# Performance work log

Hardware: AMD Instinct MI355X
Metric: run time of the kernel (lower is better)

## Reference

```python
import jax, jax.numpy as jnp
import numpy as np

DIM = 128
HEADS = 4
POS_DIM = (DIM // 4) // 4  # DynamicPosBias: pos_dim = (dim//4)//4 = 8


def _layernorm(x, g, b, eps=1e-5):
    m = x.mean(-1, keepdims=True)
    v = x.var(-1, keepdims=True)
    return (x - m) / jnp.sqrt(v + eps) * g + b


def setup_inputs() -> dict:
    key = jax.random.key(0)
    ks = jax.random.split(key, 16)
    B_, N, C = 64, 512, DIM
    s = 0.02
    inp = {
        "x": jax.random.normal(ks[0], (B_, N, C), jnp.float32),
        "y": jax.random.normal(ks[1], (B_, N, C), jnp.float32),
        "H": 8, "W": 8, "D": 8,
        "qkv_w": jax.random.normal(ks[2], (3 * C, C), jnp.float32) * s,
        "qkv_b": jnp.zeros((3 * C,), jnp.float32),
        "proj_w": jax.random.normal(ks[3], (C, C), jnp.float32) * s,
        "proj_b": jnp.zeros((C,), jnp.float32),
        "pos_proj_w": jax.random.normal(ks[4], (POS_DIM, 3), jnp.float32) * s,
        "pos_proj_b": jnp.zeros((POS_DIM,), jnp.float32),
        "ln1_g": jnp.ones((POS_DIM,), jnp.float32),
        "ln1_b": jnp.zeros((POS_DIM,), jnp.float32),
        "p1_w": jax.random.normal(ks[5], (POS_DIM, POS_DIM), jnp.float32) * s,
        "p1_b": jnp.zeros((POS_DIM,), jnp.float32),
        "ln2_g": jnp.ones((POS_DIM,), jnp.float32),
        "ln2_b": jnp.zeros((POS_DIM,), jnp.float32),
        "p2_w": jax.random.normal(ks[6], (POS_DIM, POS_DIM), jnp.float32) * s,
        "p2_b": jnp.zeros((POS_DIM,), jnp.float32),
        "ln3_g": jnp.ones((POS_DIM,), jnp.float32),
        "ln3_b": jnp.zeros((POS_DIM,), jnp.float32),
        "p3_w": jax.random.normal(ks[7], (HEADS, POS_DIM), jnp.float32) * s,
        "p3_b": jnp.zeros((HEADS,), jnp.float32),
    }
    return inp


def _rel_pos_static(H, W, D):
    # biases table: all relative offsets, shape ((2H-1)(2W-1)(2D-1), 3)
    bh = np.arange(1 - H, H)
    bw = np.arange(1 - W, W)
    bd = np.arange(1 - D, D)
    biases = np.stack(np.meshgrid(bh, bw, bd, indexing="ij")).reshape(3, -1).T
    # relative position index, shape (N, N)
    coords = np.stack(np.meshgrid(np.arange(H), np.arange(W), np.arange(D), indexing="ij")).reshape(3, -1)
    rel = coords[:, :, None] - coords[:, None, :]  # (3, N, N)
    rel = rel.transpose(1, 2, 0).astype(np.int64)
    rel[:, :, 0] += H - 1
    rel[:, :, 1] += W - 1
    rel[:, :, 2] += D - 1
    rel[:, :, 0] *= (2 * W - 1) * (2 * D - 1)
    rel[:, :, 1] *= 2 * D - 1
    idx = rel.sum(-1)  # (N, N)
    return jnp.asarray(biases, jnp.float32), jnp.asarray(idx)


def reference(x, y, H, W, D, qkv_w, qkv_b, proj_w, proj_b,
              pos_proj_w, pos_proj_b, ln1_g, ln1_b, p1_w, p1_b,
              ln2_g, ln2_b, p2_w, p2_b, ln3_g, ln3_b, p3_w, p3_b):
    B_, N, C = x.shape
    h = p3_b.shape[0]
    hd = C // h
    scale = hd ** -0.5

    def qkv_fn(t):
        q3 = (t @ qkv_w.T + qkv_b).reshape(B_, N, 3, h, hd)
        q3 = q3.transpose(2, 0, 3, 1, 4)  # (3, B, h, N, hd)
        return q3[0], q3[1], q3[2]

    q, k, v = qkv_fn(x)
    # NOTE: original code uses self.qkv(y) (not qkv_y) -- reproduced faithfully
    q_y, k_y, v_y = qkv_fn(y)

    attn = jnp.einsum("bhnd,bhmd->bhnm", q * scale, k_y)  # (B, h, N, N)

    biases, idx = _rel_pos_static(H, W, D)
    # DynamicPosBias, residual=False: pos3(pos2(pos1(pos_proj(b))))
    pos = biases @ pos_proj_w.T + pos_proj_b
    pos = jax.nn.relu(_layernorm(pos, ln1_g, ln1_b)) @ p1_w.T + p1_b
    pos = jax.nn.relu(_layernorm(pos, ln2_g, ln2_b)) @ p2_w.T + p2_b
    pos = jax.nn.relu(_layernorm(pos, ln3_g, ln3_b)) @ p3_w.T + p3_b  # (table, h)
    rpb = pos[idx.reshape(-1)].reshape(N, N, h).transpose(2, 0, 1)  # (h, N, N)

    attn = jax.nn.softmax(attn + rpb[None], axis=-1)
    out = jnp.einsum("bhnm,bhmd->bhnd", attn, v_y)
    out = out.transpose(0, 2, 1, 3).reshape(B_, N, C)
    out = out @ proj_w.T + proj_b
    return out
```

## Files before the change

### kernel.cpp

```cpp
#include <hip/hip_runtime.h>
#include <hip/hip_bf16.h>

typedef __attribute__((ext_vector_type(4))) float f32x4;
typedef __attribute__((ext_vector_type(8))) short bf16x8;
typedef __attribute__((ext_vector_type(4))) short bf16x4;
typedef __attribute__((ext_vector_type(2))) unsigned int u32x2;

#define DEV static __device__ __forceinline__

constexpr float LOG2E  = 1.4426950408889634f;
constexpr float QSCALE = 0.17677669529663687f * LOG2E;

constexpr size_t OFF_Q   = 0;
constexpr size_t OFF_K   = (size_t)8  << 20;
constexpr size_t OFF_V   = (size_t)16 << 20;
constexpr size_t OFF_RPB = (size_t)24 << 20;
constexpr size_t OFF_AO  = (size_t)27 << 20;
constexpr size_t OFF_POS = (size_t)35 << 20;
constexpr size_t OFF_WQ  = (size_t)36 << 20;
constexpr size_t OFF_WP  = (size_t)37 << 20;

DEV short f2b(float f) {
  union { __bf16 h; short s; } u;
  u.h = (__bf16)f;
  return u.s;
}
DEV float b2f(unsigned int u) {
  union { unsigned int u; float f; } x; x.u = u; return x.f;
}
DEV unsigned int pkbf(float a, float b) {
  union { __bf16 h; unsigned short s; } ua, ub;
  ua.h = (__bf16)a; ub.h = (__bf16)b;
  return (unsigned int)ua.s | ((unsigned int)ub.s << 16);
}

DEV void ln_relu8(const float* v, const float* __restrict__ g,
                  const float* __restrict__ b, float* t) {
  float m = 0.f;
#pragma unroll
  for (int i = 0; i < 8; i++) m += v[i];
  m *= 0.125f;
  float var = 0.f;
#pragma unroll
  for (int i = 0; i < 8; i++) { float d = v[i] - m; var += d * d; }
  var *= 0.125f;
  float inv = 1.0f / sqrtf(var + 1e-5f);
#pragma unroll
  for (int i = 0; i < 8; i++) {
    float u = (v[i] - m) * inv * g[i] + b[i];
    t[i] = u > 0.f ? u : 0.f;
  }
}

DEV void mm8(const float* t, const float* __restrict__ w,
             const float* __restrict__ c, float* o) {
#pragma unroll
  for (int oo = 0; oo < 8; oo++) {
    float a = c[oo];
#pragma unroll
    for (int i = 0; i < 8; i++) a += t[i] * w[oo * 8 + i];
    o[oo] = a;
  }
}

__global__ void ca_setup(
    const float* __restrict__ qkv_w, const float* __restrict__ proj_w,
    short* __restrict__ wq, short* __restrict__ wp,
    const float* __restrict__ pw, const float* __restrict__ pb,
    const float* __restrict__ g1, const float* __restrict__ b1,
    const float* __restrict__ w1, const float* __restrict__ c1,
    const float* __restrict__ g2, const float* __restrict__ b2,
    const float* __restrict__ w2, const float* __restrict__ c2,
    const float* __restrict__ g3, const float* __restrict__ b3,
    const float* __restrict__ w3, const float* __restrict__ c3,
    float* __restrict__ pos_out) {
  const int blk = blockIdx.x;
  if (blk < 256) {
    int i = blk * 256 + threadIdx.x;
    if (i < 49152) {
      float f = qkv_w[i];
      if (i < 16384) f *= QSCALE;
      wq[i] = f2b(f);
    } else {
      int j = i - 49152;
      wp[j] = f2b(proj_w[j]);
    }
    return;
  }
  int r = (blk - 256) * 256 + threadIdx.x;
  if (r >= 3375) return;
  float x0 = (float)(r / 225 - 7);
  float x1 = (float)((r / 15) % 15 - 7);
  float x2 = (float)(r % 15 - 7);
  float v[8], t[8], u[8];
#pragma unroll
  for (int o = 0; o < 8; o++)
    v[o] = x0 * pw[o * 3] + x1 * pw[o * 3 + 1] + x2 * pw[o * 3 + 2] + pb[o];
  ln_relu8(v, g1, b1, t);
  mm8(t, w1, c1, u);
  ln_relu8(u, g2, b2, t);
  mm8(t, w2, c2, v);
  ln_relu8(v, g3, b3, t);
#pragma unroll
  for (int hh = 0; hh < 4; hh++) {
    float a = c3[hh];
#pragma unroll
    for (int i = 0; i < 8; i++) a += t[i] * w3[hh * 8 + i];
    pos_out[r * 4 + hh] = a * LOG2E;
  }
}

__global__ void ca_rpb(const float* __restrict__ pos, short* __restrict__ rpbf) {
  int gid = blockIdx.x * 256 + threadIdx.x;
  int lane = gid & 63, jc = (gid >> 6) & 31, qg = (gid >> 11) & 31, hh = gid >> 16;
  int q = qg * 16 + (lane & 15);
  int j0 = jc * 16 + (lane >> 4) * 4;
  bf16x4 outv;
#pragma unroll
  for (int r = 0; r < 4; r++) {
    int j = j0 + r;
    int rh = (q >> 6) - (j >> 6) + 7;
    int rw = ((q >> 3) & 7) - ((j >> 3) & 7) + 7;
    int rd = (q & 7) - (j & 7) + 7;
    int idx = (rh * 15 + rw) * 15 + rd;
    outv[r] = f2b(pos[idx * 4 + hh]);
  }
  *(bf16x4*)(rpbf + (size_t)gid * 4) = outv;
}

__global__ __launch_bounds__(256) void ca_qkv(
    const float* __restrict__ x, const float* __restrict__ y,
    const short* __restrict__ wq, const float* __restrict__ qkv_b,
    short* __restrict__ gq, short* __restrict__ gk, short* __restrict__ gv) {
  __shared__ short lds[16384];
  const int z = blockIdx.y;
  const int t0 = blockIdx.x * 64;
  const int b_ = t0 >> 9;
  const int n0 = t0 & 511;
  const int tid = threadIdx.x;
  const float* __restrict__ in = (z == 0) ? x : y;
#pragma unroll
  for (int i = 0; i < 8; i++) {
    int flat = i * 1024 + tid * 4;
    f32x4 f = *(const f32x4*)(in + (size_t)t0 * 128 + flat);
    int row = flat >> 7, col = flat & 127;
    bf16x4 hv;
#pragma unroll
    for (int e = 0; e < 4; e++) hv[e] = f2b(f[e]);
    *(bf16x4*)(lds + row * 136 + col) = hv;
  }
  __syncthreads();
  const int w = tid >> 6, lane = tid & 63, lr = lane & 15, lg = lane >> 4;
  bf16x8 afrag[4];
  {
    const short* ap = lds + (w * 16 + lr) * 136 + lg * 8;
#pragma unroll
    for (int k4 = 0; k4 < 4; k4++) afrag[k4] = *(const bf16x8*)(ap + k4 * 32);
  }
  __syncthreads();

  const int nct = z ? 16 : 8;
  for (int ct = 0; ct < nct; ct++) {
    const int col = z * 128 + ct * 16;
    float bias = qkv_b[col + lr];
    if (z == 0) bias *= QSCALE;
    f32x4 acc = {bias, bias, bias, bias};
    const short* bp = wq + (size_t)(col + lr) * 128 + lg * 8;
#pragma unroll
    for (int k4 = 0; k4 < 4; k4++) {
      bf16x8 bfr = *(const bf16x8*)(bp + k4 * 32);
      acc = __builtin_amdgcn_mfma_f32_16x16x32_bf16(afrag[k4], bfr, acc, 0, 0, 0);
    }
    if (z == 1 && ct >= 8) {
      const int hv_ = (ct - 8) >> 1;
      const int dh = (ct - 8) & 1;
      const int base = 8192 + (((hv_ * 2 + (w >> 1)) * 2 + dh) * 512) + lane * 8 + (w & 1) * 4;
      *(unsigned int*)(lds + base)     = pkbf(acc[0], acc[1]);
      *(unsigned int*)(lds + base + 2) = pkbf(acc[2], acc[3]);
    } else {
      const int d = (ct & 1) * 16 + lr;
      const int base = (w * 4 + (ct >> 1)) * 512 + 128 * (d >> 3) + (d & 7);
#pragma unroll
      for (int r = 0; r < 4; r++)
        lds[base + (lg * 4 + r) * 8] = f2b(acc[r]);
    }
  }
  __syncthreads();
  if (z == 0) {
#pragma unroll
    for (int kk = 0; kk < 4; kk++) {
      const int c = kk * 4 + w, hh = c & 3, tg = c >> 2;
      bf16x8 vd = *(const bf16x8*)(lds + c * 512 + lane * 8);
      *(bf16x8*)(gq + (((size_t)b_ * 4 + hh) * 32 + (n0 >> 4) + tg) * 512 + lane * 8) = vd;
    }
  } else {
#pragma unroll
    for (int kk = 0; kk < 4; kk++) {
      const int c = kk * 4 + w, hh = c & 3, tg = c >> 2;
      bf16x8 vd = *(const bf16x8*)(lds + c * 512 + lane * 8);
      *(bf16x8*)(gk + (((size_t)b_ * 4 + hh) * 32 + (n0 >> 4) + tg) * 512 + lane * 8) = vd;
    }
#pragma unroll
    for (int kk = 0; kk < 4; kk++) {
      const int c = kk * 4 + w, hh = c >> 2, ul = (c >> 1) & 1, dh = c & 1;
      bf16x8 vd = *(const bf16x8*)(lds + 8192 + c * 512 + lane * 8);
      *(bf16x8*)(gv + ((((size_t)b_ * 4 + hh) * 16 + (n0 >> 5) + ul) * 2 + dh) * 512 + lane * 8) = vd;
    }
  }
}

DEV void stage_kv(const short* kg, const short* vg, short* buf, int T, int w, int lane) {
#pragma unroll
  for (int i = 0; i < 4; i++) {
    const int c = w * 4 + i;
    const short* src;
    short* dst;
    if (c < 8) {
      src = kg + ((size_t)(T * 8 + c)) * 512 + lane * 8;
      dst = buf + c * 512;
    } else {
      src = vg + ((size_t)(T * 8 + c - 8)) * 512 + lane * 8;
      dst = buf + 4096 + (c - 8) * 512;
    }
    __builtin_amdgcn_global_load_lds((const __attribute__((address_space(1))) void*)src,
                                     (__attribute__((address_space(3))) void*)dst, 16, 0, 0);
  }
}

__global__ __launch_bounds__(256, 4) void ca_attn(
    const short* __restrict__ qfrag, const short* __restrict__ kfrag,
    const short* __restrict__ vfrag, const short* __restrict__ rpbf,
    short* __restrict__ aob) {
  __shared__ short kv[2][8192];
  const int bid = blockIdx.x;
  const int qt = bid >> 8, rem = bid & 255;
  const int b_ = rem >> 2, hh = rem & 3;
  const int bh = b_ * 4 + hh;
  const int tid = threadIdx.x;
  const int w = tid >> 6, lane = tid & 63, lg = lane >> 4;
  const int q0 = qt * 64 + w * 16, qg = (q0 >> 4);

  const short* kg = kfrag + (size_t)bh * 16384;
  const short* vg = vfrag + (size_t)bh * 16384;
  const bf16x8 qf = *(const bf16x8*)(qfrag + ((size_t)bh * 32 + qg) * 512 + lane * 8);
  const short* bp = rpbf + ((size_t)(hh * 32 + qg) << 13) + lane * 4;

  union PU { bf16x8 v; unsigned int u[4]; };
  PU ones;
  ones.u[0] = 0x3F803F80u; ones.u[1] = 0x3F803F80u;
  ones.u[2] = 0x3F803F80u; ones.u[3] = 0x3F803F80u;

  stage_kv(kg, vg, &kv[0][0], 0, w, lane);
  __syncthreads();

  f32x4 o0 = {0.f, 0.f, 0.f, 0.f}, o1 = {0.f, 0.f, 0.f, 0.f}, o2 = {0.f, 0.f, 0.f, 0.f};

  for (int T = 0; T < 4; T++) {
    const int cur = T & 1;
    if (T < 3) stage_kv(kg, vg, &kv[cur ^ 1][0], T + 1, w, lane);
    const short* kt = &kv[cur][0];
    const short* vt = &kv[cur][4096];

    u32x2 bw[8];
#pragma unroll
    for (int t = 0; t < 8; t++) bw[t] = *(const u32x2*)(bp + (size_t)(T * 8 + t) * 256);

#pragma unroll
    for (int uu = 0; uu < 4; uu++) {
      PU p;
#pragma unroll
      for (int half = 0; half < 2; half++) {
        const int t = uu * 2 + half;
        bf16x8 kf = *(const bf16x8*)(kt + t * 512 + lane * 8);
        f32x4 cin;
        cin[0] = b2f(bw[t].x << 16);
        cin[1] = b2f(bw[t].x & 0xFFFF0000u);
        cin[2] = b2f(bw[t].y << 16);
        cin[3] = b2f(bw[t].y & 0xFFFF0000u);
        f32x4 s = __builtin_amdgcn_mfma_f32_16x16x32_bf16(kf, qf, cin, 0, 0, 0);
        p.u[half * 2 + 0] = pkbf(__builtin_exp2f(s[0]), __builtin_exp2f(s[1]));
        p.u[half * 2 + 1] = pkbf(__builtin_exp2f(s[2]), __builtin_exp2f(s[3]));
      }
      bf16x8 vf0 = *(const bf16x8*)(vt + (uu * 2 + 0) * 512 + lane * 8);
      bf16x8 vf1 = *(const bf16x8*)(vt + (uu * 2 + 1) * 512 + lane * 8);
      o0 = __builtin_amdgcn_mfma_f32_16x16x32_bf16(p.v, vf0, o0, 0, 0, 0);
      o1 = __builtin_amdgcn_mfma_f32_16x16x32_bf16(p.v, vf1, o1, 0, 0, 0);
      o2 = __builtin_amdgcn_mfma_f32_16x16x32_bf16(p.v, ones.v, o2, 0, 0, 0);
    }
    if (T < 3) __syncthreads();
  }

  short* pt = &kv[0][w * 1024];
  const int lr = lane & 15;
#pragma unroll
  for (int r = 0; r < 4; r++) {
    float iv = 1.0f / o2[r];
    pt[(lg * 4 + r) * 40 + lr] = f2b(o0[r] * iv);
    pt[(lg * 4 + r) * 40 + 16 + lr] = f2b(o1[r] * iv);
  }
  asm volatile("s_waitcnt lgkmcnt(0)" ::: "memory");
  __builtin_amdgcn_sched_barrier(0);
  {
    const int qq = lane >> 2, pp = lane & 3;
    bf16x8 od = *(const bf16x8*)(pt + qq * 40 + pp * 8);
    *(bf16x8*)(aob + ((size_t)bh * 512 + q0 + qq) * 32 + pp * 8) = od;
  }
}

__global__ __launch_bounds__(256) void ca_proj(
    const short* __restrict__ aob, const short* __restrict__ wp,
    const float* __restrict__ proj_b, float* __restrict__ out) {
  const int t0 = blockIdx.x * 64;
  const int b_ = t0 >> 9, n0 = t0 & 511;
  const int tid = threadIdx.x;
  const int w = tid >> 6, lane = tid & 63, lr = lane & 15, lg = lane >> 4;
  bf16x8 afrag[4];
#pragma unroll
  for (int k4 = 0; k4 < 4; k4++)
    afrag[k4] = *(const bf16x8*)(aob + (((size_t)b_ * 4 + k4) * 512 + n0 + w * 16 + lr) * 32 + lg * 8);
#pragma unroll
  for (int ct = 0; ct < 8; ct++) {
    float bias = proj_b[ct * 16 + lr];
    f32x4 acc = {bias, bias, bias, bias};
    const short* bp = wp + (size_t)(ct * 16 + lr) * 128 + lg * 8;
#pragma unroll
    for (int k4 = 0; k4 < 4; k4++) {
      bf16x8 bfr = *(const bf16x8*)(bp + k4 * 32);
      acc = __builtin_amdgcn_mfma_f32_16x16x32_bf16(afrag[k4], bfr, acc, 0, 0, 0);
    }
#pragma unroll
    for (int r = 0; r < 4; r++)
      out[(size_t)(t0 + w * 16 + lg * 4 + r) * 128 + ct * 16 + lr] = acc[r];
  }
}

extern "C" void kernel_launch(void* const* d_in, const int* in_sizes, int n_in,
                              void* d_out, int out_size, void* d_ws, size_t ws_size,
                              hipStream_t stream) {
  const float* x      = (const float*)d_in[0];
  const float* y      = (const float*)d_in[1];
  const float* qkv_w  = (const float*)d_in[5];
  const float* qkv_b  = (const float*)d_in[6];
  const float* proj_w = (const float*)d_in[7];
  const float* proj_b = (const float*)d_in[8];
  const float* pos_w  = (const float*)d_in[9];
  const float* pos_b  = (const float*)d_in[10];
  const float* ln1g = (const float*)d_in[11];
  const float* ln1b = (const float*)d_in[12];
  const float* p1w  = (const float*)d_in[13];
  const float* p1b  = (const float*)d_in[14];
  const float* ln2g = (const float*)d_in[15];
  const float* ln2b = (const float*)d_in[16];
  const float* p2w  = (const float*)d_in[17];
  const float* p2b  = (const float*)d_in[18];
  const float* ln3g = (const float*)d_in[19];
  const float* ln3b = (const float*)d_in[20];
  const float* p3w  = (const float*)d_in[21];
  const float* p3b  = (const float*)d_in[22];
  float* out = (float*)d_out;

  char* ws = (char*)d_ws;
  short* gq    = (short*)(ws + OFF_Q);
  short* gk    = (short*)(ws + OFF_K);
  short* gv    = (short*)(ws + OFF_V);
  short* rpbf  = (short*)(ws + OFF_RPB);
  short* aob   = (short*)(ws + OFF_AO);
  float* posb  = (float*)(ws + OFF_POS);
  short* wq    = (short*)(ws + OFF_WQ);
  short* wp    = (short*)(ws + OFF_WP);

  ca_setup<<<270, 256, 0, stream>>>(qkv_w, proj_w, wq, wp,
                                    pos_w, pos_b, ln1g, ln1b, p1w, p1b,
                                    ln2g, ln2b, p2w, p2b, ln3g, ln3b, p3w, p3b, posb);
  ca_rpb<<<1024, 256, 0, stream>>>(posb, rpbf);
  ca_qkv<<<dim3(512, 2), 256, 0, stream>>>(x, y, wq, qkv_b, gq, gk, gv);
  ca_attn<<<2048, 256, 0, stream>>>(gq, gk, gv, rpbf, aob);
  ca_proj<<<512, 256, 0, stream>>>(aob, wp, proj_b, out);
}
```

Before: 84.36 us.

## Process two query groups per wave in attention to reuse K/V tiles

Each attention wave now handles two 16-row query groups (qg0 and qg0+4), so every K and V fragment read from LDS feeds two MFMAs, and the grid shrinks from 2048 to 1024 blocks. This halves K/V staging and LDS traffic per query, at the cost of more registers per wave and less parallelism. The PV MFMAs are wrapped in s_setprio so the matrix phase gets issue priority. The weight bf16 conversion moves from the pos-MLP setup kernel into the rpb kernel, leaving the pos-MLP kernel with only 14 blocks that may finish sooner.

```diff
diff --git a/kernel.cpp b/kernel.cpp
--- a/kernel.cpp
+++ b/kernel.cpp
@@ -63,9 +63,7 @@
   }
 }
 
-__global__ void ca_setup(
-    const float* __restrict__ qkv_w, const float* __restrict__ proj_w,
-    short* __restrict__ wq, short* __restrict__ wp,
+__global__ void ca_posmlp(
     const float* __restrict__ pw, const float* __restrict__ pb,
     const float* __restrict__ g1, const float* __restrict__ b1,
     const float* __restrict__ w1, const float* __restrict__ c1,
@@ -74,20 +72,7 @@
     const float* __restrict__ g3, const float* __restrict__ b3,
     const float* __restrict__ w3, const float* __restrict__ c3,
     float* __restrict__ pos_out) {
-  const int blk = blockIdx.x;
-  if (blk < 256) {
-    int i = blk * 256 + threadIdx.x;
-    if (i < 49152) {
-      float f = qkv_w[i];
-      if (i < 16384) f *= QSCALE;
-      wq[i] = f2b(f);
-    } else {
-      int j = i - 49152;
-      wp[j] = f2b(proj_w[j]);
-    }
-    return;
-  }
-  int r = (blk - 256) * 256 + threadIdx.x;
+  int r = blockIdx.x * 256 + threadIdx.x;
   if (r >= 3375) return;
   float x0 = (float)(r / 225 - 7);
   float x1 = (float)((r / 15) % 15 - 7);
@@ -110,8 +95,22 @@
   }
 }
 
-__global__ void ca_rpb(const float* __restrict__ pos, short* __restrict__ rpbf) {
-  int gid = blockIdx.x * 256 + threadIdx.x;
+__global__ void ca_rpbw(const float* __restrict__ pos, short* __restrict__ rpbf,
+                        const float* __restrict__ qkv_w, const float* __restrict__ proj_w,
+                        short* __restrict__ wq, short* __restrict__ wp) {
+  const int blk = blockIdx.x;
+  if (blk >= 1024) {
+    int i = (blk - 1024) * 256 + threadIdx.x;
+    if (i < 49152) {
+      float f = qkv_w[i];
+      if (i < 16384) f *= QSCALE;
+      wq[i] = f2b(f);
+    } else {
+      wp[i - 49152] = f2b(proj_w[i - 49152]);
+    }
+    return;
+  }
+  int gid = blk * 256 + threadIdx.x;
   int lane = gid & 63, jc = (gid >> 6) & 31, qg = (gid >> 11) & 31, hh = gid >> 16;
   int q = qg * 16 + (lane & 15);
   int j0 = jc * 16 + (lane >> 4) * 4;
@@ -233,17 +232,20 @@
     short* __restrict__ aob) {
   __shared__ short kv[2][8192];
   const int bid = blockIdx.x;
-  const int qt = bid >> 8, rem = bid & 255;
+  const int qt2 = bid >> 8, rem = bid & 255;
   const int b_ = rem >> 2, hh = rem & 3;
   const int bh = b_ * 4 + hh;
   const int tid = threadIdx.x;
   const int w = tid >> 6, lane = tid & 63, lg = lane >> 4;
-  const int q0 = qt * 64 + w * 16, qg = (q0 >> 4);
+  const int qg0 = qt2 * 8 + w, qg1 = qg0 + 4;
+  const int q0 = qg0 * 16;
 
   const short* kg = kfrag + (size_t)bh * 16384;
   const short* vg = vfrag + (size_t)bh * 16384;
-  const bf16x8 qf = *(const bf16x8*)(qfrag + ((size_t)bh * 32 + qg) * 512 + lane * 8);
-  const short* bp = rpbf + ((size_t)(hh * 32 + qg) << 13) + lane * 4;
+  const bf16x8 qf0 = *(const bf16x8*)(qfrag + ((size_t)bh * 32 + qg0) * 512 + lane * 8);
+  const bf16x8 qf1 = *(const bf16x8*)(qfrag + ((size_t)bh * 32 + qg1) * 512 + lane * 8);
+  const short* bp0 = rpbf + ((size_t)(hh * 32 + qg0) << 13) + lane * 4;
+  const short* bp1 = rpbf + ((size_t)(hh * 32 + qg1) << 13) + lane * 4;
 
   union PU { bf16x8 v; unsigned int u[4]; };
   PU ones;
@@ -253,7 +255,8 @@
   stage_kv(kg, vg, &kv[0][0], 0, w, lane);
   __syncthreads();
 
-  f32x4 o0 = {0.f, 0.f, 0.f, 0.f}, o1 = {0.f, 0.f, 0.f, 0.f}, o2 = {0.f, 0.f, 0.f, 0.f};
+  f32x4 a0 = {0.f, 0.f, 0.f, 0.f}, a1 = {0.f, 0.f, 0.f, 0.f}, a2 = {0.f, 0.f, 0.f, 0.f};
+  f32x4 b0 = {0.f, 0.f, 0.f, 0.f}, b1 = {0.f, 0.f, 0.f, 0.f}, b2 = {0.f, 0.f, 0.f, 0.f};
 
   for (int T = 0; T < 4; T++) {
     const int cur = T & 1;
@@ -261,49 +264,70 @@
     const short* kt = &kv[cur][0];
     const short* vt = &kv[cur][4096];
 
-    u32x2 bw[8];
-#pragma unroll
-    for (int t = 0; t < 8; t++) bw[t] = *(const u32x2*)(bp + (size_t)(T * 8 + t) * 256);
+    u32x2 bw0[8], bw1[8];
+#pragma unroll
+    for (int t = 0; t < 8; t++) {
+      bw0[t] = *(const u32x2*)(bp0 + (size_t)(T * 8 + t) * 256);
+      bw1[t] = *(const u32x2*)(bp1 + (size_t)(T * 8 + t) * 256);
+    }
 
 #pragma unroll
     for (int uu = 0; uu < 4; uu++) {
-      PU p;
+      PU p0, p1;
 #pragma unroll
       for (int half = 0; half < 2; half++) {
         const int t = uu * 2 + half;
         bf16x8 kf = *(const bf16x8*)(kt + t * 512 + lane * 8);
-        f32x4 cin;
-        cin[0] = b2f(bw[t].x << 16);
-        cin[1] = b2f(bw[t].x & 0xFFFF0000u);
-        cin[2] = b2f(bw[t].y << 16);
-        cin[3] = b2f(bw[t].y & 0xFFFF0000u);
-        f32x4 s = __builtin_amdgcn_mfma_f32_16x16x32_bf16(kf, qf, cin, 0, 0, 0);
-        p.u[half * 2 + 0] = pkbf(__builtin_exp2f(s[0]), __builtin_exp2f(s[1]));
-        p.u[half * 2 + 1] = pkbf(__builtin_exp2f(s[2]), __builtin_exp2f(s[3]));
+        f32x4 c0, c1;
+        c0[0] = b2f(bw0[t].x << 16);
+        c0[1] = b2f(bw0[t].x & 0xFFFF0000u);
+        c0[2] = b2f(bw0[t].y << 16);
+        c0[3] = b2f(bw0[t].y & 0xFFFF0000u);
+        c1[0] = b2f(bw1[t].x << 16);
+        c1[1] = b2f(bw1[t].x & 0xFFFF0000u);
+        c1[2] = b2f(bw1[t].y << 16);
+        c1[3] = b2f(bw1[t].y & 0xFFFF0000u);
+        f32x4 s0 = __builtin_amdgcn_mfma_f32_16x16x32_bf16(kf, qf0, c0, 0, 0, 0);
+        f32x4 s1 = __builtin_amdgcn_mfma_f32_16x16x32_bf16(kf, qf1, c1, 0, 0, 0);
+        p0.u[half * 2 + 0] = pkbf(__builtin_exp2f(s0[0]), __builtin_exp2f(s0[1]));
+        p0.u[half * 2 + 1] = pkbf(__builtin_exp2f(s0[2]), __builtin_exp2f(s0[3]));
+        p1.u[half * 2 + 0] = pkbf(__builtin_exp2f(s1[0]), __builtin_exp2f(s1[1]));
+        p1.u[half * 2 + 1] = pkbf(__builtin_exp2f(s1[2]), __builtin_exp2f(s1[3]));
       }
       bf16x8 vf0 = *(const bf16x8*)(vt + (uu * 2 + 0) * 512 + lane * 8);
       bf16x8 vf1 = *(const bf16x8*)(vt + (uu * 2 + 1) * 512 + lane * 8);
-      o0 = __builtin_amdgcn_mfma_f32_16x16x32_bf16(p.v, vf0, o0, 0, 0, 0);
-      o1 = __builtin_amdgcn_mfma_f32_16x16x32_bf16(p.v, vf1, o1, 0, 0, 0);
-      o2 = __builtin_amdgcn_mfma_f32_16x16x32_bf16(p.v, ones.v, o2, 0, 0, 0);
+      __builtin_amdgcn_s_setprio(1);
+      a0 = __builtin_amdgcn_mfma_f32_16x16x32_bf16(p0.v, vf0, a0, 0, 0, 0);
+      a1 = __builtin_amdgcn_mfma_f32_16x16x32_bf16(p0.v, vf1, a1, 0, 0, 0);
+      a2 = __builtin_amdgcn_mfma_f32_16x16x32_bf16(p0.v, ones.v, a2, 0, 0, 0);
+      b0 = __builtin_amdgcn_mfma_f32_16x16x32_bf16(p1.v, vf0, b0, 0, 0, 0);
+      b1 = __builtin_amdgcn_mfma_f32_16x16x32_bf16(p1.v, vf1, b1, 0, 0, 0);
+      b2 = __builtin_amdgcn_mfma_f32_16x16x32_bf16(p1.v, ones.v, b2, 0, 0, 0);
+      __builtin_amdgcn_s_setprio(0);
     }
     if (T < 3) __syncthreads();
   }
 
-  short* pt = &kv[0][w * 1024];
   const int lr = lane & 15;
+  short* pt0 = &kv[0][(w * 2 + 0) * 1024];
+  short* pt1 = &kv[0][(w * 2 + 1) * 1024];
 #pragma unroll
   for (int r = 0; r < 4; r++) {
-    float iv = 1.0f / o2[r];
-    pt[(lg * 4 + r) * 40 + lr] = f2b(o0[r] * iv);
-    pt[(lg * 4 + r) * 40 + 16 + lr] = f2b(o1[r] * iv);
+    float iv = 1.0f / a2[r];
+    pt0[(lg * 4 + r) * 40 + lr] = f2b(a0[r] * iv);
+    pt0[(lg * 4 + r) * 40 + 16 + lr] = f2b(a1[r] * iv);
+    float jv = 1.0f / b2[r];
+    pt1[(lg * 4 + r) * 40 + lr] = f2b(b0[r] * jv);
+    pt1[(lg * 4 + r) * 40 + 16 + lr] = f2b(b1[r] * jv);
   }
   asm volatile("s_waitcnt lgkmcnt(0)" ::: "memory");
   __builtin_amdgcn_sched_barrier(0);
   {
     const int qq = lane >> 2, pp = lane & 3;
-    bf16x8 od = *(const bf16x8*)(pt + qq * 40 + pp * 8);
-    *(bf16x8*)(aob + ((size_t)bh * 512 + q0 + qq) * 32 + pp * 8) = od;
+    bf16x8 od0 = *(const bf16x8*)(pt0 + qq * 40 + pp * 8);
+    bf16x8 od1 = *(const bf16x8*)(pt1 + qq * 40 + pp * 8);
+    *(bf16x8*)(aob + ((size_t)bh * 512 + q0 + qq) * 32 + pp * 8) = od0;
+    *(bf16x8*)(aob + ((size_t)bh * 512 + q0 + 64 + qq) * 32 + pp * 8) = od1;
   }
 }
 
@@ -369,11 +393,10 @@
   short* wq    = (short*)(ws + OFF_WQ);
   short* wp    = (short*)(ws + OFF_WP);
 
-  ca_setup<<<270, 256, 0, stream>>>(qkv_w, proj_w, wq, wp,
-                                    pos_w, pos_b, ln1g, ln1b, p1w, p1b,
+  ca_posmlp<<<14, 256, 0, stream>>>(pos_w, pos_b, ln1g, ln1b, p1w, p1b,
                                     ln2g, ln2b, p2w, p2b, ln3g, ln3b, p3w, p3b, posb);
-  ca_rpb<<<1024, 256, 0, stream>>>(posb, rpbf);
+  ca_rpbw<<<1280, 256, 0, stream>>>(posb, rpbf, qkv_w, proj_w, wq, wp);
   ca_qkv<<<dim3(512, 2), 256, 0, stream>>>(x, y, wq, qkv_b, gq, gk, gv);
-  ca_attn<<<2048, 256, 0, stream>>>(gq, gk, gv, rpbf, aob);
+  ca_attn<<<1024, 256, 0, stream>>>(gq, gk, gv, rpbf, aob);
   ca_proj<<<512, 256, 0, stream>>>(aob, wp, proj_b, out);
 }
```

After: 85.73 us. About the same (+1.6%).

## Stage proj output through LDS, split qkv z-paths, move weight cast into rpb kernel

Applied to the files above, without the earlier changes.

The projection kernel now writes its MFMA results into padded shared memory and then issues coalesced 16-byte row stores, replacing scattered 4-byte global stores. The qkv kernel splits the z==0 and z==1 column loops into separate fully unrolled branches, removing the per-iteration branch on z. The bf16 weight conversion moves from the small pos-MLP setup kernel into the rpb kernel as extra blocks, so the tiny pos MLP launch stays short. The proj change adds about 33 KB of LDS per block, which may lower occupancy.

```diff
diff --git a/kernel.cpp b/kernel.cpp
--- a/kernel.cpp
+++ b/kernel.cpp
@@ -63,9 +63,7 @@
   }
 }
 
-__global__ void ca_setup(
-    const float* __restrict__ qkv_w, const float* __restrict__ proj_w,
-    short* __restrict__ wq, short* __restrict__ wp,
+__global__ void ca_posmlp(
     const float* __restrict__ pw, const float* __restrict__ pb,
     const float* __restrict__ g1, const float* __restrict__ b1,
     const float* __restrict__ w1, const float* __restrict__ c1,
@@ -74,20 +72,7 @@
     const float* __restrict__ g3, const float* __restrict__ b3,
     const float* __restrict__ w3, const float* __restrict__ c3,
     float* __restrict__ pos_out) {
-  const int blk = blockIdx.x;
-  if (blk < 256) {
-    int i = blk * 256 + threadIdx.x;
-    if (i < 49152) {
-      float f = qkv_w[i];
-      if (i < 16384) f *= QSCALE;
-      wq[i] = f2b(f);
-    } else {
-      int j = i - 49152;
-      wp[j] = f2b(proj_w[j]);
-    }
-    return;
-  }
-  int r = (blk - 256) * 256 + threadIdx.x;
+  int r = blockIdx.x * 256 + threadIdx.x;
   if (r >= 3375) return;
   float x0 = (float)(r / 225 - 7);
   float x1 = (float)((r / 15) % 15 - 7);
@@ -110,8 +95,22 @@
   }
 }
 
-__global__ void ca_rpb(const float* __restrict__ pos, short* __restrict__ rpbf) {
-  int gid = blockIdx.x * 256 + threadIdx.x;
+__global__ void ca_rpbw(const float* __restrict__ pos, short* __restrict__ rpbf,
+                        const float* __restrict__ qkv_w, const float* __restrict__ proj_w,
+                        short* __restrict__ wq, short* __restrict__ wp) {
+  const int blk = blockIdx.x;
+  if (blk >= 1024) {
+    int i = (blk - 1024) * 256 + threadIdx.x;
+    if (i < 49152) {
+      float f = qkv_w[i];
+      if (i < 16384) f *= QSCALE;
+      wq[i] = f2b(f);
+    } else {
+      wp[i - 49152] = f2b(proj_w[i - 49152]);
+    }
+    return;
+  }
+  int gid = blk * 256 + threadIdx.x;
   int lane = gid & 63, jc = (gid >> 6) & 31, qg = (gid >> 11) & 31, hh = gid >> 16;
   int q = qg * 16 + (lane & 15);
   int j0 = jc * 16 + (lane >> 4) * 4;
@@ -159,30 +158,49 @@
   }
   __syncthreads();
 
-  const int nct = z ? 16 : 8;
-  for (int ct = 0; ct < nct; ct++) {
-    const int col = z * 128 + ct * 16;
-    float bias = qkv_b[col + lr];
-    if (z == 0) bias *= QSCALE;
-    f32x4 acc = {bias, bias, bias, bias};
-    const short* bp = wq + (size_t)(col + lr) * 128 + lg * 8;
-#pragma unroll
-    for (int k4 = 0; k4 < 4; k4++) {
-      bf16x8 bfr = *(const bf16x8*)(bp + k4 * 32);
-      acc = __builtin_amdgcn_mfma_f32_16x16x32_bf16(afrag[k4], bfr, acc, 0, 0, 0);
-    }
-    if (z == 1 && ct >= 8) {
-      const int hv_ = (ct - 8) >> 1;
-      const int dh = (ct - 8) & 1;
-      const int base = 8192 + (((hv_ * 2 + (w >> 1)) * 2 + dh) * 512) + lane * 8 + (w & 1) * 4;
-      *(unsigned int*)(lds + base)     = pkbf(acc[0], acc[1]);
-      *(unsigned int*)(lds + base + 2) = pkbf(acc[2], acc[3]);
-    } else {
+  if (z == 0) {
+#pragma unroll
+    for (int ct = 0; ct < 8; ct++) {
+      const int col = ct * 16;
+      float bias = qkv_b[col + lr] * QSCALE;
+      f32x4 acc = {bias, bias, bias, bias};
+      const short* bp = wq + (size_t)(col + lr) * 128 + lg * 8;
+#pragma unroll
+      for (int k4 = 0; k4 < 4; k4++) {
+        bf16x8 bfr = *(const bf16x8*)(bp + k4 * 32);
+        acc = __builtin_amdgcn_mfma_f32_16x16x32_bf16(afrag[k4], bfr, acc, 0, 0, 0);
+      }
       const int d = (ct & 1) * 16 + lr;
       const int base = (w * 4 + (ct >> 1)) * 512 + 128 * (d >> 3) + (d & 7);
 #pragma unroll
       for (int r = 0; r < 4; r++)
         lds[base + (lg * 4 + r) * 8] = f2b(acc[r]);
+    }
+  } else {
+#pragma unroll
+    for (int ct = 0; ct < 16; ct++) {
+      const int col = 128 + ct * 16;
+      float bias = qkv_b[col + lr];
+      f32x4 acc = {bias, bias, bias, bias};
+      const short* bp = wq + (size_t)(col + lr) * 128 + lg * 8;
+#pragma unroll
+      for (int k4 = 0; k4 < 4; k4++) {
+        bf16x8 bfr = *(const bf16x8*)(bp + k4 * 32);
+        acc = __builtin_amdgcn_mfma_f32_16x16x32_bf16(afrag[k4], bfr, acc, 0, 0, 0);
+      }
+      if (ct >= 8) {
+        const int hv_ = (ct - 8) >> 1;
+        const int dh = (ct - 8) & 1;
+        const int base = 8192 + (((hv_ * 2 + (w >> 1)) * 2 + dh) * 512) + lane * 8 + (w & 1) * 4;
+        *(unsigned int*)(lds + base)     = pkbf(acc[0], acc[1]);
+        *(unsigned int*)(lds + base + 2) = pkbf(acc[2], acc[3]);
+      } else {
+        const int d = (ct & 1) * 16 + lr;
+        const int base = (w * 4 + (ct >> 1)) * 512 + 128 * (d >> 3) + (d & 7);
+#pragma unroll
+        for (int r = 0; r < 4; r++)
+          lds[base + (lg * 4 + r) * 8] = f2b(acc[r]);
+      }
     }
   }
   __syncthreads();
@@ -310,6 +328,7 @@
 __global__ __launch_bounds__(256) void ca_proj(
     const short* __restrict__ aob, const short* __restrict__ wp,
     const float* __restrict__ proj_b, float* __restrict__ out) {
+  __shared__ float plds[8448];
   const int t0 = blockIdx.x * 64;
   const int b_ = t0 >> 9, n0 = t0 & 511;
   const int tid = threadIdx.x;
@@ -318,6 +337,7 @@
 #pragma unroll
   for (int k4 = 0; k4 < 4; k4++)
     afrag[k4] = *(const bf16x8*)(aob + (((size_t)b_ * 4 + k4) * 512 + n0 + w * 16 + lr) * 32 + lg * 8);
+  float* pt = plds + w * 2112;
 #pragma unroll
   for (int ct = 0; ct < 8; ct++) {
     float bias = proj_b[ct * 16 + lr];
@@ -330,7 +350,16 @@
     }
 #pragma unroll
     for (int r = 0; r < 4; r++)
-      out[(size_t)(t0 + w * 16 + lg * 4 + r) * 128 + ct * 16 + lr] = acc[r];
+      pt[(lg * 4 + r) * 132 + ct * 16 + lr] = acc[r];
+  }
+  asm volatile("s_waitcnt lgkmcnt(0)" ::: "memory");
+  __builtin_amdgcn_sched_barrier(0);
+#pragma unroll
+  for (int i = 0; i < 8; i++) {
+    int f = i * 256 + lane * 4;
+    int row = f >> 7, col = f & 127;
+    f32x4 v = *(const f32x4*)(pt + row * 132 + col);
+    *(f32x4*)(out + (size_t)(t0 + w * 16) * 128 + f) = v;
   }
 }
 
@@ -369,10 +398,9 @@
   short* wq    = (short*)(ws + OFF_WQ);
   short* wp    = (short*)(ws + OFF_WP);
 
-  ca_setup<<<270, 256, 0, stream>>>(qkv_w, proj_w, wq, wp,
-                                    pos_w, pos_b, ln1g, ln1b, p1w, p1b,
+  ca_posmlp<<<14, 256, 0, stream>>>(pos_w, pos_b, ln1g, ln1b, p1w, p1b,
                                     ln2g, ln2b, p2w, p2b, ln3g, ln3b, p3w, p3b, posb);
-  ca_rpb<<<1024, 256, 0, stream>>>(posb, rpbf);
+  ca_rpbw<<<1280, 256, 0, stream>>>(posb, rpbf, qkv_w, proj_w, wq, wp);
   ca_qkv<<<dim3(512, 2), 256, 0, stream>>>(x, y, wq, qkv_b, gq, gk, gv);
   ca_attn<<<2048, 256, 0, stream>>>(gq, gk, gv, rpbf, aob);
   ca_proj<<<512, 256, 0, stream>>>(aob, wp, proj_b, out);
```

After: 83.56 us. No clear change (-1.0%).
